# Performance work log

Hardware: AMD Instinct MI355X
Metric: run time of the kernel (lower is better)

Reference implementation:

```python
import jax, jax.numpy as jnp
import numpy as np

B, C, H, W = 16, 512, 32, 32
NUM_GROUPS = 32
EPS = 1e-5


def setup_inputs() -> dict:
    key = jax.random.key(0)
    ks = jax.random.split(key, 7)
    x = jax.random.normal(ks[0], (B, C, H, W), dtype=jnp.float32)
    gamma = jnp.ones((C,), dtype=jnp.float32)
    beta = jnp.zeros((C,), dtype=jnp.float32)
    # project_in: Conv2d(C, 3C, 1) -> weight [3C, C], bias [3C]
    w_in = jax.random.normal(ks[1], (3 * C, C), dtype=jnp.float32) / np.sqrt(C)
    b_in = jnp.zeros((3 * C,), dtype=jnp.float32)
    # project_out: Conv2d(C, C, 1) with init_scale=0.0 -> zero-init in original;
    # use small random weights so gradients/outputs are non-trivial for testing.
    w_out = jax.random.normal(ks[2], (C, C), dtype=jnp.float32) / np.sqrt(C)
    b_out = jnp.zeros((C,), dtype=jnp.float32)
    return {"x": x, "gamma": gamma, "beta": beta, "w_in": w_in, "b_in": b_in,
            "w_out": w_out, "b_out": b_out}


def group_norm(x, gamma, beta):
    b, c, h, w = x.shape
    xg = x.reshape(b, NUM_GROUPS, c // NUM_GROUPS, h, w)
    mean = xg.mean(axis=(2, 3, 4), keepdims=True)
    var = xg.var(axis=(2, 3, 4), keepdims=True)
    xn = ((xg - mean) * jax.lax.rsqrt(var + EPS)).reshape(b, c, h, w)
    return xn * gamma[None, :, None, None] + beta[None, :, None, None]


def reference(x, gamma, beta, w_in, b_in, w_out, b_out):
    skip = x  # in_channels == out_channels -> Identity skip
    xn = group_norm(x, gamma, beta)
    # 1x1 conv == channel matmul
    qkv = jnp.einsum('oc,bchw->bohw', w_in, xn) + b_in[None, :, None, None]
    q, k, v = jnp.split(qkv, 3, axis=1)  # each [B, C, H, W]
    cm = q.shape[1]
    # [B, H, W, H*W] scores
    scores = jnp.einsum('bchw,bcHW->bhwHW', q, k).reshape(B, H, W, H * W)
    attn = jax.nn.softmax(scores / jnp.sqrt(jnp.float32(cm)), axis=-1)
    attn = attn.reshape(B, H, W, H, W)
    out = jnp.einsum('bhwHW,bcHW->bchw', attn, v)
    out = jnp.einsum('oc,bchw->bohw', w_out, out) + b_out[None, :, None, None]
    return out + skip
```

## Files before the change

kernel.cpp:

```cpp
#include <hip/hip_runtime.h>
#include <hip/hip_bf16.h>
#include <cstdint>
#include <cstddef>

#define HW   1024
#define NC   512
#define NB   16
#define EPSV 1e-5f

typedef __hip_bfloat16 bf16;
typedef __attribute__((ext_vector_type(8))) __bf16 bf16x8;
typedef __attribute__((ext_vector_type(4))) float f32x4;

__device__ __forceinline__ float b2f(bf16 h) { return __bfloat162float(h); }

__device__ __forceinline__ void gload16(const void* g, void* l) {
  __builtin_amdgcn_global_load_lds(
      (const __attribute__((address_space(1))) uint32_t*)g,
      (__attribute__((address_space(3))) uint32_t*)l, 16, 0, 0);
}

__global__ __launch_bounds__(256) void cvt_w_kernel(
    const float* __restrict__ wi, const float* __restrict__ wo,
    bf16* __restrict__ wib, bf16* __restrict__ wob) {
  int i = blockIdx.x * 256 + threadIdx.x;
  const float4* src;
  bf16* dst;
  int j;
  if (i < 196608) { src = (const float4*)wi; j = i; dst = wib; }
  else            { src = (const float4*)wo; j = i - 196608; dst = wob; }
  float4 v = src[j];
  union { bf16 h[4]; uint2 u; } p;
  p.h[0] = __float2bfloat16(v.x); p.h[1] = __float2bfloat16(v.y);
  p.h[2] = __float2bfloat16(v.z); p.h[3] = __float2bfloat16(v.w);
  *(uint2*)&dst[(size_t)j * 4] = p.u;
}

__global__ __launch_bounds__(256) void gn_kernel(
    const float* __restrict__ x, const float* __restrict__ gamma,
    const float* __restrict__ beta, bf16* __restrict__ xn) {
  int blk = blockIdx.x;
  int b = blk >> 5, g = blk & 31;
  size_t base = ((size_t)(b * NC + g * 16)) * HW;
  const float4* src4 = (const float4*)(x + base);
  int t = threadIdx.x;
  float s = 0.f, ss = 0.f;
  float4 v[16];
#pragma unroll
  for (int i = 0; i < 16; ++i) {
    v[i] = src4[t + i * 256];
    s  += v[i].x + v[i].y + v[i].z + v[i].w;
    ss += v[i].x * v[i].x + v[i].y * v[i].y + v[i].z * v[i].z + v[i].w * v[i].w;
  }
  __shared__ float red[256];
  red[t] = s; __syncthreads();
  for (int o = 128; o > 0; o >>= 1) { if (t < o) red[t] += red[t + o]; __syncthreads(); }
  float mean = red[0] * (1.f / 16384.f);
  __syncthreads();
  red[t] = ss; __syncthreads();
  for (int o = 128; o > 0; o >>= 1) { if (t < o) red[t] += red[t + o]; __syncthreads(); }
  float var = red[0] * (1.f / 16384.f) - mean * mean;
  float rstd = rsqrtf(var + EPSV);

  __shared__ bf16 sm[16][1032];
#pragma unroll
  for (int i = 0; i < 16; ++i) {
    int idx = t + i * 256;
    int c = idx >> 8;
    int hw4 = (idx & 255) * 4;
    float gm = gamma[g * 16 + c], bt = beta[g * 16 + c];
    union { bf16 h[4]; uint2 u; } p;
    p.h[0] = __float2bfloat16((v[i].x - mean) * rstd * gm + bt);
    p.h[1] = __float2bfloat16((v[i].y - mean) * rstd * gm + bt);
    p.h[2] = __float2bfloat16((v[i].z - mean) * rstd * gm + bt);
    p.h[3] = __float2bfloat16((v[i].w - mean) * rstd * gm + bt);
    *(uint2*)&sm[c][hw4] = p.u;
  }
  __syncthreads();
  bf16* dst = xn + (size_t)b * HW * NC + g * 16;
#pragma unroll
  for (int it = 0; it < 8; ++it) {
    int u = it * 256 + t;
    int hw = u >> 1;
    int c8 = (u & 1) * 8;
    union { bf16 h[8]; uint4 q; } p;
#pragma unroll
    for (int j = 0; j < 8; ++j) p.h[j] = sm[c8 + j][hw];
    *(uint4*)&dst[(size_t)hw * NC + c8] = p.q;
  }
}

template <int MODE>
__global__ __launch_bounds__(256) void gemm_bt(
    const bf16* __restrict__ A, int lda, long long sA,
    const bf16* __restrict__ B, int ldb, long long sB,
    void* __restrict__ Cv, int ldc, long long sC,
    int K,
    const float* __restrict__ bias) {
  __shared__ bf16 sT[2][128][32];
  int z = blockIdx.z;
  const bf16* Ab = A + (size_t)z * sA;
  const bf16* Bb = B + (size_t)z * sB;
  int n0 = blockIdx.x * 128, m0 = blockIdx.y * 128;
  int t = threadIdx.x;
  int l = t & 63, w = t >> 6;
  int wm = w >> 1, wn = w & 1;

  int srow = t >> 2;
  int scol = (t & 3) * 8;

  f32x4 acc[4][4] = {};

  const bf16* ga0 = Ab + (size_t)(m0 + srow) * lda + scol;
  const bf16* gb0 = Bb + (size_t)(n0 + srow) * ldb + scol;

  for (int k0 = 0; k0 < K; k0 += 32) {
    gload16(ga0 + k0, &sT[0][srow][scol]);
    gload16(ga0 + (size_t)64 * lda + k0, &sT[0][64 + srow][scol]);
    gload16(gb0 + k0, &sT[1][srow][scol]);
    gload16(gb0 + (size_t)64 * ldb + k0, &sT[1][64 + srow][scol]);
    __syncthreads();
    bf16x8 af[4], bfr[4];
    int kc = (l >> 4) * 8;
    int ra = wm * 64 + (l & 15);
    int rb = wn * 64 + (l & 15);
#pragma unroll
    for (int i = 0; i < 4; ++i) {
      af[i]  = *(const bf16x8*)&sT[0][ra + i * 16][kc];
      bfr[i] = *(const bf16x8*)&sT[1][rb + i * 16][kc];
    }
#pragma unroll
    for (int i = 0; i < 4; ++i)
#pragma unroll
      for (int j = 0; j < 4; ++j)
        acc[i][j] = __builtin_amdgcn_mfma_f32_16x16x32_bf16(af[i], bfr[j], acc[i][j], 0, 0, 0);
    __syncthreads();
  }

  int rbase = (l >> 4) * 4;
#pragma unroll
  for (int i = 0; i < 4; ++i) {
    int row = m0 + wm * 64 + i * 16 + rbase;
    float4 bv = make_float4(0.f, 0.f, 0.f, 0.f);
    if (MODE == 0) bv = *(const float4*)&bias[row];
    else if (MODE == 1) { if (bias) bv = *(const float4*)&bias[row]; }
#pragma unroll
    for (int j = 0; j < 4; ++j) {
      int col = n0 + wn * 64 + j * 16 + (l & 15);
      if (MODE == 0) {
        bf16* C = (bf16*)Cv + (size_t)z * sC;
        union { bf16 h[4]; uint2 u; } p;
        p.h[0] = __float2bfloat16(acc[i][j][0] + bv.x);
        p.h[1] = __float2bfloat16(acc[i][j][1] + bv.y);
        p.h[2] = __float2bfloat16(acc[i][j][2] + bv.z);
        p.h[3] = __float2bfloat16(acc[i][j][3] + bv.w);
        *(uint2*)&C[(size_t)col * ldc + row] = p.u;
      } else {
        bf16* C = (bf16*)Cv + (size_t)z * sC;
        float bb[4] = {bv.x, bv.y, bv.z, bv.w};
#pragma unroll
        for (int r = 0; r < 4; ++r)
          C[(size_t)(row + r) * ldc + col] = __float2bfloat16(acc[i][j][r] + bb[r]);
      }
    }
  }
}

__global__ __launch_bounds__(512, 1) void flash_kernel(
    const bf16* __restrict__ qk, const bf16* __restrict__ vcm,
    const bf16* __restrict__ wout, const float* __restrict__ b_out,
    const float* __restrict__ x, float* __restrict__ out) {
  __shared__ char lds[163840];
  char* Qs  = lds;
  char* Kb0 = lds + 65536;
  char* Kb1 = lds + 81920;
  char* Vs  = lds + 98304;
  char* Wb0 = lds + 65536;
  char* Wb1 = lds + 98304;
  float* redl = (float*)(lds + 131072);

  int id = blockIdx.x;
  int xcd = id & 7, rest = id >> 3;
  int q = rest & 15, bh = rest >> 4;
  int b = xcd + bh * 8;
  int i0 = q * 64;

  const char* qkC = (const char*)qk + (size_t)b * 2097152;
  const char* vC  = (const char*)vcm + (size_t)b * 1048576;
  const char* wC  = (const char*)wout;

  int t = threadIdx.x, l = t & 63, w = t >> 6;
  int l15 = l & 15, lq = l >> 4;
  int jg = w >> 1, ih = w & 1;
  int chb = w * 64;

  auto stage_k = [&](int tile_, int p_, char* dst_) {
#pragma unroll
    for (int qq = 0; qq < 2; ++qq) {
      int A = qq * 8192 + t * 16;
      int jh = A >> 12, k2 = (A >> 10) & 3, jlo = (A >> 6) & 15, cb = A & 63;
      gload16(qkC + (size_t)(tile_ * 64 + jh * 16 + jlo) * 2048 + 1024
                  + p_ * 256 + k2 * 64 + cb,
              dst_ + A);
    }
  };
  auto stage_v = [&](int tile_, int v_) {
    int chh = t >> 7, js = (t >> 6) & 1, cl = (t >> 2) & 15, jb = (t & 3) * 16;
    int ch = v_ * 64 + chh * 16 + cl;
    gload16(vC + (size_t)ch * 2048 + tile_ * 128 + js * 64 + jb,
            Vs + v_ * 8192 + t * 16);
  };
  auto stage_w = [&](int kc_, char* dst_) {
#pragma unroll
    for (int it = 0; it < 4; ++it) {
      int A = it * 8192 + t * 16;
      int coh = A >> 10, col = (A >> 6) & 15, cb = A & 63;
      gload16(wC + (size_t)(coh * 16 + col) * 1024 + kc_ * 64 + cb, dst_ + A);
    }
  };

  {
#pragma unroll
    for (int it = 0; it < 8; ++it) {
      int A = it * 8192 + t * 16;
      int ih2 = A >> 14, ks = (A >> 10) & 15, ilo = (A >> 6) & 15, cb = A & 63;
      gload16(qkC + (size_t)(i0 + ih2 * 16 + ilo) * 2048 + ks * 64 + cb, Qs + A);
    }
  }
  stage_k(0, 0, Kb0);

  float lacc[2] = {0.f, 0.f};
  f32x4 o[4][4] = {};
  const float scl = 0.044194173824159216f;

  __syncthreads();

  for (int tile = 0; tile < 16; ++tile) {
    char* PsBuf = (tile & 1) ? Kb1 : Kb0;
    f32x4 s[2] = {};
#pragma unroll
    for (int p = 0; p < 4; ++p) {
      if (p < 3) {
        char* kd = ((p + 1 + tile) & 1) ? Kb1 : Kb0;
        stage_k(tile, p + 1, kd);
      }
      stage_v(tile, p * 2);
      stage_v(tile, p * 2 + 1);
      const char* kcur = ((p + tile) & 1) ? Kb1 : Kb0;
#pragma unroll
      for (int k2 = 0; k2 < 4; ++k2) {
        bf16x8 kf = *(const bf16x8*)(kcur + jg * 4096 + k2 * 1024 + l15 * 64 + lq * 16);
#pragma unroll
        for (int ni = 0; ni < 2; ++ni) {
          bf16x8 qf = *(const bf16x8*)(Qs + (ih * 2 + ni) * 16384
                        + (p * 4 + k2) * 1024 + l15 * 64 + lq * 16);
          s[ni] = __builtin_amdgcn_mfma_f32_16x16x32_bf16(kf, qf, s[ni], 0, 0, 0);
        }
      }
      __syncthreads();
    }
#pragma unroll
    for (int ni = 0; ni < 2; ++ni) {
      int i = ih * 32 + ni * 16 + l15;
      float p0 = __expf(s[ni][0] * scl);
      float p1 = __expf(s[ni][1] * scl);
      float p2 = __expf(s[ni][2] * scl);
      float p3 = __expf(s[ni][3] * scl);
      lacc[ni] += p0 + p1 + p2 + p3;
      union { bf16 h[4]; uint64_t u; } pk;
      pk.h[0] = __float2bfloat16(p0); pk.h[1] = __float2bfloat16(p1);
      pk.h[2] = __float2bfloat16(p2); pk.h[3] = __float2bfloat16(p3);
      int dst = (ih * 2 + ni) * 2048 + (jg >> 1) * 1024 + l15 * 64
              + (jg & 1) * 32 + lq * 8;
      *(uint64_t*)(PsBuf + dst) = pk.u;
      (void)i;
    }
    __syncthreads();
    if (tile < 15) {
      char* kd = ((tile + 1) & 1) ? Kb1 : Kb0;
      stage_k(tile + 1, 0, kd);
    }
#pragma unroll
    for (int ks = 0; ks < 2; ++ks) {
      bf16x8 vf[4];
#pragma unroll
      for (int mi = 0; mi < 4; ++mi)
        vf[mi] = *(const bf16x8*)(Vs + (w * 4 + mi) * 2048 + ks * 1024
                   + l15 * 64 + lq * 16);
#pragma unroll
      for (int ni = 0; ni < 4; ++ni) {
        bf16x8 pf = *(const bf16x8*)(PsBuf + ni * 2048 + ks * 1024
                      + l15 * 64 + lq * 16);
#pragma unroll
        for (int mi = 0; mi < 4; ++mi)
          o[mi][ni] = __builtin_amdgcn_mfma_f32_16x16x32_bf16(vf[mi], pf, o[mi][ni], 0, 0, 0);
      }
    }
    __syncthreads();
  }

  stage_w(0, Wb0);
#pragma unroll
  for (int ni = 0; ni < 2; ++ni) {
    float v = lacc[ni];
    v += __shfl_xor(v, 16);
    v += __shfl_xor(v, 32);
    if (l < 16) redl[jg * 64 + ih * 32 + ni * 16 + l] = v;
  }
  __syncthreads();
  float linv[4];
#pragma unroll
  for (int ni = 0; ni < 4; ++ni) {
    int i = ni * 16 + l15;
    linv[ni] = 1.f / (redl[i] + redl[64 + i] + redl[128 + i] + redl[192 + i]);
  }
#pragma unroll
  for (int mi = 0; mi < 4; ++mi)
#pragma unroll
    for (int ni = 0; ni < 4; ++ni) {
      union { bf16 h[4]; uint64_t u; } pk;
#pragma unroll
      for (int r = 0; r < 4; ++r)
        pk.h[r] = __float2bfloat16(o[mi][ni][r] * linv[ni]);
      int dst = ni * 16384 + (w * 2 + (mi >> 1)) * 1024 + l15 * 64
              + (mi & 1) * 32 + lq * 8;
      *(uint64_t*)(Qs + dst) = pk.u;
    }
  __syncthreads();

  f32x4 acc2[4][4] = {};
#pragma unroll
  for (int kc = 0; kc < 16; ++kc) {
    if (kc < 15) stage_w(kc + 1, ((kc + 1) & 1) ? Wb1 : Wb0);
    const char* Wc = (kc & 1) ? Wb1 : Wb0;
    bf16x8 wf[4];
#pragma unroll
    for (int mi = 0; mi < 4; ++mi)
      wf[mi] = *(const bf16x8*)(Wc + (w * 4 + mi) * 1024 + l15 * 64 + lq * 16);
#pragma unroll
    for (int ni = 0; ni < 4; ++ni) {
      bf16x8 pf = *(const bf16x8*)(Qs + ni * 16384 + kc * 1024
                    + l15 * 64 + lq * 16);
#pragma unroll
      for (int mi = 0; mi < 4; ++mi)
        acc2[mi][ni] = __builtin_amdgcn_mfma_f32_16x16x32_bf16(wf[mi], pf, acc2[mi][ni], 0, 0, 0);
    }
    __syncthreads();
  }

  const float* xb = x + (size_t)b * 524288;
  float* ob = out + (size_t)b * 524288;
#pragma unroll
  for (int mi = 0; mi < 4; ++mi) {
    int cbase = chb + mi * 16 + lq * 4;
    float4 bv = *(const float4*)&b_out[cbase];
    float bb[4] = {bv.x, bv.y, bv.z, bv.w};
#pragma unroll
    for (int ni = 0; ni < 4; ++ni) {
      int i = i0 + ni * 16 + l15;
#pragma unroll
      for (int r = 0; r < 4; ++r) {
        size_t off = (size_t)(cbase + r) * 1024 + i;
        ob[off] = acc2[mi][ni][r] + bb[r] + xb[off];
      }
    }
  }
}

extern "C" void kernel_launch(void* const* d_in, const int* in_sizes, int n_in,
                              void* d_out, int out_size, void* d_ws, size_t ws_size,
                              hipStream_t stream) {
  const float* x     = (const float*)d_in[0];
  const float* gamma = (const float*)d_in[1];
  const float* beta  = (const float*)d_in[2];
  const float* w_in  = (const float*)d_in[3];
  const float* b_in  = (const float*)d_in[4];
  const float* w_out = (const float*)d_in[5];
  const float* b_out = (const float*)d_in[6];
  float* out = (float*)d_out;

  char* w = (char*)d_ws;
  bf16* xn  = (bf16*)w;
  bf16* qk  = (bf16*)(w + ((size_t)16 << 20));
  bf16* vcm = (bf16*)(w + ((size_t)48 << 20));
  bf16* wib = (bf16*)(w + ((size_t)64 << 20));
  bf16* wob = (bf16*)(w + ((size_t)64 << 20) + ((size_t)3 << 19));

  cvt_w_kernel<<<1024, 256, 0, stream>>>(w_in, w_out, wib, wob);
  gn_kernel<<<NB * 32, 256, 0, stream>>>(x, gamma, beta, xn);

  gemm_bt<0><<<dim3(8, 8, NB), 256, 0, stream>>>(
      wib, 512, 0, xn, 512, 512 * 1024, qk, 1024, 1024 * 1024, 512, b_in);
  gemm_bt<1><<<dim3(8, 4, NB), 256, 0, stream>>>(
      wib + 1024 * 512, 512, 0, xn, 512, 512 * 1024, vcm, 1024, 512 * 1024, 512,
      b_in + 1024);

  flash_kernel<<<256, 512, 0, stream>>>(qk, vcm, wob, b_out, x, out);
}
```

Baseline: 151.7 us.

## Pre-swizzle K, V and W_out into MFMA fragment layouts and load them directly

The QKV projection epilogues now write K, V and the converted output-projection weight straight into MFMA-fragment-ordered layouts. The attention kernel can then read operand fragments from global memory into registers instead of staging them through LDS with barriers. The key loop is reorganised into 8 tiles of 128 keys, with each wave owning one 16-key slice, and LDS use drops from 160KB to 96KB. The cost is uncoalesced scattered stores in the GEMM epilogues (MODE 5 writes single bf16 elements) and reliance on cache/latency hiding for direct global fragment loads in the hot loop.

```diff
diff --git a/kernel.cpp b/kernel.cpp
--- a/kernel.cpp
+++ b/kernel.cpp
@@ -12,8 +12,6 @@
 typedef __attribute__((ext_vector_type(8))) __bf16 bf16x8;
 typedef __attribute__((ext_vector_type(4))) float f32x4;
 
-__device__ __forceinline__ float b2f(bf16 h) { return __bfloat162float(h); }
-
 __device__ __forceinline__ void gload16(const void* g, void* l) {
   __builtin_amdgcn_global_load_lds(
       (const __attribute__((address_space(1))) uint32_t*)g,
@@ -22,18 +20,25 @@
 
 __global__ __launch_bounds__(256) void cvt_w_kernel(
     const float* __restrict__ wi, const float* __restrict__ wo,
-    bf16* __restrict__ wib, bf16* __restrict__ wob) {
+    bf16* __restrict__ wib, char* __restrict__ wobf) {
   int i = blockIdx.x * 256 + threadIdx.x;
-  const float4* src;
-  bf16* dst;
-  int j;
-  if (i < 196608) { src = (const float4*)wi; j = i; dst = wib; }
-  else            { src = (const float4*)wo; j = i - 196608; dst = wob; }
-  float4 v = src[j];
-  union { bf16 h[4]; uint2 u; } p;
-  p.h[0] = __float2bfloat16(v.x); p.h[1] = __float2bfloat16(v.y);
-  p.h[2] = __float2bfloat16(v.z); p.h[3] = __float2bfloat16(v.w);
-  *(uint2*)&dst[(size_t)j * 4] = p.u;
+  if (i < 196608) {
+    float4 v = ((const float4*)wi)[i];
+    union { bf16 h[4]; uint2 u; } p;
+    p.h[0] = __float2bfloat16(v.x); p.h[1] = __float2bfloat16(v.y);
+    p.h[2] = __float2bfloat16(v.z); p.h[3] = __float2bfloat16(v.w);
+    *(uint2*)&wib[(size_t)i * 4] = p.u;
+  } else {
+    int j = i - 196608;
+    float4 v = ((const float4*)wo)[j];
+    int elem = j * 4;
+    int co = elem >> 9, c = elem & 511;
+    union { bf16 h[4]; uint2 u; } p;
+    p.h[0] = __float2bfloat16(v.x); p.h[1] = __float2bfloat16(v.y);
+    p.h[2] = __float2bfloat16(v.z); p.h[3] = __float2bfloat16(v.w);
+    int chh = co >> 4, col_ = co & 15, kc = c >> 5, cc = c & 31;
+    *(uint2*)(wobf + (((chh * 16 + kc) << 10) + col_ * 64 + cc * 2)) = p.u;
+  }
 }
 
 __global__ __launch_bounds__(256) void gn_kernel(
@@ -141,43 +146,50 @@
 #pragma unroll
   for (int i = 0; i < 4; ++i) {
     int row = m0 + wm * 64 + i * 16 + rbase;
-    float4 bv = make_float4(0.f, 0.f, 0.f, 0.f);
-    if (MODE == 0) bv = *(const float4*)&bias[row];
-    else if (MODE == 1) { if (bias) bv = *(const float4*)&bias[row]; }
+    float4 bv = *(const float4*)&bias[row];
+    float bb[4] = {bv.x, bv.y, bv.z, bv.w};
 #pragma unroll
     for (int j = 0; j < 4; ++j) {
       int col = n0 + wn * 64 + j * 16 + (l & 15);
       if (MODE == 0) {
         bf16* C = (bf16*)Cv + (size_t)z * sC;
         union { bf16 h[4]; uint2 u; } p;
-        p.h[0] = __float2bfloat16(acc[i][j][0] + bv.x);
-        p.h[1] = __float2bfloat16(acc[i][j][1] + bv.y);
-        p.h[2] = __float2bfloat16(acc[i][j][2] + bv.z);
-        p.h[3] = __float2bfloat16(acc[i][j][3] + bv.w);
+#pragma unroll
+        for (int r = 0; r < 4; ++r) p.h[r] = __float2bfloat16(acc[i][j][r] + bb[r]);
         *(uint2*)&C[(size_t)col * ldc + row] = p.u;
+      } else if (MODE == 4) {
+        char* C = (char*)Cv + (size_t)z * sC * 2;
+        int tile = col >> 7, jgc = (col >> 4) & 7, j_lo = col & 15;
+        int kw = row >> 5, cc = row & 31;
+        union { bf16 h[4]; uint2 u; } p;
+#pragma unroll
+        for (int r = 0; r < 4; ++r) p.h[r] = __float2bfloat16(acc[i][j][r] + bb[r]);
+        *(uint2*)(C + (((tile * 8 + jgc) * 16 + kw) << 10) + j_lo * 64 + cc * 2) = p.u;
       } else {
-        bf16* C = (bf16*)Cv + (size_t)z * sC;
-        float bb[4] = {bv.x, bv.y, bv.z, bv.w};
-#pragma unroll
-        for (int r = 0; r < 4; ++r)
-          C[(size_t)(row + r) * ldc + col] = __float2bfloat16(acc[i][j][r] + bb[r]);
+        char* C = (char*)Cv + (size_t)z * sC * 2;
+        int tile = col >> 7, jj = col & 127;
+        int ks = jj >> 5, jc = jj & 31;
+#pragma unroll
+        for (int r = 0; r < 4; ++r) {
+          int ch = row + r;
+          int chh = ch >> 4, chl = ch & 15;
+          *(bf16*)(C + (((tile * 32 + chh) * 4 + ks) << 10)
+                     + chl * 64 + jc * 2) = __float2bfloat16(acc[i][j][r] + bb[r]);
+        }
       }
     }
   }
 }
 
 __global__ __launch_bounds__(512, 1) void flash_kernel(
-    const bf16* __restrict__ qk, const bf16* __restrict__ vcm,
-    const bf16* __restrict__ wout, const float* __restrict__ b_out,
-    const float* __restrict__ x, float* __restrict__ out) {
-  __shared__ char lds[163840];
-  char* Qs  = lds;
-  char* Kb0 = lds + 65536;
-  char* Kb1 = lds + 81920;
-  char* Vs  = lds + 98304;
-  char* Wb0 = lds + 65536;
-  char* Wb1 = lds + 98304;
-  float* redl = (float*)(lds + 131072);
+    const bf16* __restrict__ qtok, const bf16* __restrict__ kfrag,
+    const bf16* __restrict__ vfrag, const bf16* __restrict__ wfrag,
+    const float* __restrict__ b_out, const float* __restrict__ x,
+    float* __restrict__ out) {
+  __shared__ char lds[98304];
+  char* Qs = lds;
+  char* Ps = lds + 65536;
+  float* redl = (float*)(lds + 65536);
 
   int id = blockIdx.x;
   int xcd = id & 7, rest = id >> 3;
@@ -185,83 +197,51 @@
   int b = xcd + bh * 8;
   int i0 = q * 64;
 
-  const char* qkC = (const char*)qk + (size_t)b * 2097152;
-  const char* vC  = (const char*)vcm + (size_t)b * 1048576;
-  const char* wC  = (const char*)wout;
+  const char* qC = (const char*)qtok + (size_t)b * 1048576;
+  const char* kC = (const char*)kfrag + (size_t)b * 1048576;
+  const char* vC = (const char*)vfrag + (size_t)b * 1048576;
+  const char* wC = (const char*)wfrag;
 
   int t = threadIdx.x, l = t & 63, w = t >> 6;
   int l15 = l & 15, lq = l >> 4;
-  int jg = w >> 1, ih = w & 1;
+  int fofs = l15 * 64 + lq * 16;
   int chb = w * 64;
 
-  auto stage_k = [&](int tile_, int p_, char* dst_) {
-#pragma unroll
-    for (int qq = 0; qq < 2; ++qq) {
-      int A = qq * 8192 + t * 16;
-      int jh = A >> 12, k2 = (A >> 10) & 3, jlo = (A >> 6) & 15, cb = A & 63;
-      gload16(qkC + (size_t)(tile_ * 64 + jh * 16 + jlo) * 2048 + 1024
-                  + p_ * 256 + k2 * 64 + cb,
-              dst_ + A);
-    }
-  };
-  auto stage_v = [&](int tile_, int v_) {
-    int chh = t >> 7, js = (t >> 6) & 1, cl = (t >> 2) & 15, jb = (t & 3) * 16;
-    int ch = v_ * 64 + chh * 16 + cl;
-    gload16(vC + (size_t)ch * 2048 + tile_ * 128 + js * 64 + jb,
-            Vs + v_ * 8192 + t * 16);
-  };
-  auto stage_w = [&](int kc_, char* dst_) {
-#pragma unroll
-    for (int it = 0; it < 4; ++it) {
-      int A = it * 8192 + t * 16;
-      int coh = A >> 10, col = (A >> 6) & 15, cb = A & 63;
-      gload16(wC + (size_t)(coh * 16 + col) * 1024 + kc_ * 64 + cb, dst_ + A);
-    }
-  };
-
-  {
-#pragma unroll
-    for (int it = 0; it < 8; ++it) {
-      int A = it * 8192 + t * 16;
-      int ih2 = A >> 14, ks = (A >> 10) & 15, ilo = (A >> 6) & 15, cb = A & 63;
-      gload16(qkC + (size_t)(i0 + ih2 * 16 + ilo) * 2048 + ks * 64 + cb, Qs + A);
-    }
-  }
-  stage_k(0, 0, Kb0);
-
-  float lacc[2] = {0.f, 0.f};
+#pragma unroll
+  for (int it = 0; it < 8; ++it) {
+    int A = it * 8192 + t * 16;
+    int ih2 = A >> 14, ks = (A >> 10) & 15, ilo = (A >> 6) & 15, cb = A & 63;
+    gload16(qC + (size_t)(i0 + ih2 * 16 + ilo) * 1024 + ks * 64 + cb, Qs + A);
+  }
+
+  float lacc[4] = {0.f, 0.f, 0.f, 0.f};
   f32x4 o[4][4] = {};
   const float scl = 0.044194173824159216f;
 
   __syncthreads();
 
-  for (int tile = 0; tile < 16; ++tile) {
-    char* PsBuf = (tile & 1) ? Kb1 : Kb0;
-    f32x4 s[2] = {};
-#pragma unroll
-    for (int p = 0; p < 4; ++p) {
-      if (p < 3) {
-        char* kd = ((p + 1 + tile) & 1) ? Kb1 : Kb0;
-        stage_k(tile, p + 1, kd);
+  for (int tile = 0; tile < 8; ++tile) {
+    char* Pc = Ps + (tile & 1) * 16384;
+    bf16x8 vf[4][4];
+#pragma unroll
+    for (int ks = 0; ks < 4; ++ks)
+#pragma unroll
+      for (int mi = 0; mi < 4; ++mi)
+        vf[ks][mi] = *(const bf16x8*)(vC
+            + (((size_t)(tile * 32 + (w * 4 + mi)) * 4 + ks) << 10) + fofs);
+    f32x4 s[4] = {};
+#pragma unroll
+    for (int kw = 0; kw < 16; ++kw) {
+      bf16x8 kf = *(const bf16x8*)(kC
+          + (((size_t)(tile * 8 + w) * 16 + kw) << 10) + fofs);
+#pragma unroll
+      for (int ni = 0; ni < 4; ++ni) {
+        bf16x8 qf = *(const bf16x8*)(Qs + ni * 16384 + kw * 1024 + fofs);
+        s[ni] = __builtin_amdgcn_mfma_f32_16x16x32_bf16(kf, qf, s[ni], 0, 0, 0);
       }
-      stage_v(tile, p * 2);
-      stage_v(tile, p * 2 + 1);
-      const char* kcur = ((p + tile) & 1) ? Kb1 : Kb0;
-#pragma unroll
-      for (int k2 = 0; k2 < 4; ++k2) {
-        bf16x8 kf = *(const bf16x8*)(kcur + jg * 4096 + k2 * 1024 + l15 * 64 + lq * 16);
-#pragma unroll
-        for (int ni = 0; ni < 2; ++ni) {
-          bf16x8 qf = *(const bf16x8*)(Qs + (ih * 2 + ni) * 16384
-                        + (p * 4 + k2) * 1024 + l15 * 64 + lq * 16);
-          s[ni] = __builtin_amdgcn_mfma_f32_16x16x32_bf16(kf, qf, s[ni], 0, 0, 0);
-        }
-      }
-      __syncthreads();
-    }
-#pragma unroll
-    for (int ni = 0; ni < 2; ++ni) {
-      int i = ih * 32 + ni * 16 + l15;
+    }
+#pragma unroll
+    for (int ni = 0; ni < 4; ++ni) {
       float p0 = __expf(s[ni][0] * scl);
       float p1 = __expf(s[ni][1] * scl);
       float p2 = __expf(s[ni][2] * scl);
@@ -270,49 +250,37 @@
       union { bf16 h[4]; uint64_t u; } pk;
       pk.h[0] = __float2bfloat16(p0); pk.h[1] = __float2bfloat16(p1);
       pk.h[2] = __float2bfloat16(p2); pk.h[3] = __float2bfloat16(p3);
-      int dst = (ih * 2 + ni) * 2048 + (jg >> 1) * 1024 + l15 * 64
-              + (jg & 1) * 32 + lq * 8;
-      *(uint64_t*)(PsBuf + dst) = pk.u;
-      (void)i;
+      *(uint64_t*)(Pc + ni * 4096 + (w >> 1) * 1024 + l15 * 64
+                   + (w & 1) * 32 + lq * 8) = pk.u;
     }
     __syncthreads();
-    if (tile < 15) {
-      char* kd = ((tile + 1) & 1) ? Kb1 : Kb0;
-      stage_k(tile + 1, 0, kd);
-    }
-#pragma unroll
-    for (int ks = 0; ks < 2; ++ks) {
-      bf16x8 vf[4];
-#pragma unroll
-      for (int mi = 0; mi < 4; ++mi)
-        vf[mi] = *(const bf16x8*)(Vs + (w * 4 + mi) * 2048 + ks * 1024
-                   + l15 * 64 + lq * 16);
+#pragma unroll
+    for (int ks = 0; ks < 4; ++ks)
 #pragma unroll
       for (int ni = 0; ni < 4; ++ni) {
-        bf16x8 pf = *(const bf16x8*)(PsBuf + ni * 2048 + ks * 1024
-                      + l15 * 64 + lq * 16);
+        bf16x8 pf = *(const bf16x8*)(Pc + ni * 4096 + ks * 1024 + fofs);
 #pragma unroll
         for (int mi = 0; mi < 4; ++mi)
-          o[mi][ni] = __builtin_amdgcn_mfma_f32_16x16x32_bf16(vf[mi], pf, o[mi][ni], 0, 0, 0);
+          o[mi][ni] = __builtin_amdgcn_mfma_f32_16x16x32_bf16(vf[ks][mi], pf, o[mi][ni], 0, 0, 0);
       }
-    }
-    __syncthreads();
-  }
-
-  stage_w(0, Wb0);
-#pragma unroll
-  for (int ni = 0; ni < 2; ++ni) {
+  }
+
+#pragma unroll
+  for (int ni = 0; ni < 4; ++ni) {
     float v = lacc[ni];
     v += __shfl_xor(v, 16);
     v += __shfl_xor(v, 32);
-    if (l < 16) redl[jg * 64 + ih * 32 + ni * 16 + l] = v;
+    if (l < 16) redl[w * 64 + ni * 16 + l] = v;
   }
   __syncthreads();
   float linv[4];
 #pragma unroll
   for (int ni = 0; ni < 4; ++ni) {
     int i = ni * 16 + l15;
-    linv[ni] = 1.f / (redl[i] + redl[64 + i] + redl[128 + i] + redl[192 + i]);
+    float v = redl[i];
+#pragma unroll
+    for (int w2 = 1; w2 < 8; ++w2) v += redl[w2 * 64 + i];
+    linv[ni] = 1.f / v;
   }
 #pragma unroll
   for (int mi = 0; mi < 4; ++mi)
@@ -331,21 +299,17 @@
   f32x4 acc2[4][4] = {};
 #pragma unroll
   for (int kc = 0; kc < 16; ++kc) {
-    if (kc < 15) stage_w(kc + 1, ((kc + 1) & 1) ? Wb1 : Wb0);
-    const char* Wc = (kc & 1) ? Wb1 : Wb0;
     bf16x8 wf[4];
 #pragma unroll
     for (int mi = 0; mi < 4; ++mi)
-      wf[mi] = *(const bf16x8*)(Wc + (w * 4 + mi) * 1024 + l15 * 64 + lq * 16);
+      wf[mi] = *(const bf16x8*)(wC + (((size_t)(w * 4 + mi) * 16 + kc) << 10) + fofs);
 #pragma unroll
     for (int ni = 0; ni < 4; ++ni) {
-      bf16x8 pf = *(const bf16x8*)(Qs + ni * 16384 + kc * 1024
-                    + l15 * 64 + lq * 16);
+      bf16x8 pf = *(const bf16x8*)(Qs + ni * 16384 + kc * 1024 + fofs);
 #pragma unroll
       for (int mi = 0; mi < 4; ++mi)
         acc2[mi][ni] = __builtin_amdgcn_mfma_f32_16x16x32_bf16(wf[mi], pf, acc2[mi][ni], 0, 0, 0);
     }
-    __syncthreads();
   }
 
   const float* xb = x + (size_t)b * 524288;
@@ -380,20 +344,25 @@
   float* out = (float*)d_out;
 
   char* w = (char*)d_ws;
-  bf16* xn  = (bf16*)w;
-  bf16* qk  = (bf16*)(w + ((size_t)16 << 20));
-  bf16* vcm = (bf16*)(w + ((size_t)48 << 20));
-  bf16* wib = (bf16*)(w + ((size_t)64 << 20));
-  bf16* wob = (bf16*)(w + ((size_t)64 << 20) + ((size_t)3 << 19));
-
-  cvt_w_kernel<<<1024, 256, 0, stream>>>(w_in, w_out, wib, wob);
+  bf16* xn    = (bf16*)w;
+  bf16* qtok  = (bf16*)(w + ((size_t)16 << 20));
+  bf16* kfrag = (bf16*)(w + ((size_t)32 << 20));
+  bf16* vfrag = (bf16*)(w + ((size_t)48 << 20));
+  bf16* wib   = (bf16*)(w + ((size_t)64 << 20));
+  char* wobf  = (char*)(w + ((size_t)64 << 20) + ((size_t)3 << 19));
+
+  cvt_w_kernel<<<1024, 256, 0, stream>>>(w_in, w_out, wib, wobf);
   gn_kernel<<<NB * 32, 256, 0, stream>>>(x, gamma, beta, xn);
 
-  gemm_bt<0><<<dim3(8, 8, NB), 256, 0, stream>>>(
-      wib, 512, 0, xn, 512, 512 * 1024, qk, 1024, 1024 * 1024, 512, b_in);
-  gemm_bt<1><<<dim3(8, 4, NB), 256, 0, stream>>>(
-      wib + 1024 * 512, 512, 0, xn, 512, 512 * 1024, vcm, 1024, 512 * 1024, 512,
+  gemm_bt<0><<<dim3(8, 4, NB), 256, 0, stream>>>(
+      wib, 512, 0, xn, 512, 512 * 1024, qtok, 512, 512 * 1024, 512, b_in);
+  gemm_bt<4><<<dim3(8, 4, NB), 256, 0, stream>>>(
+      wib + 512 * 512, 512, 0, xn, 512, 512 * 1024, kfrag, 0, 512 * 1024, 512,
+      b_in + 512);
+  gemm_bt<5><<<dim3(8, 4, NB), 256, 0, stream>>>(
+      wib + 1024 * 512, 512, 0, xn, 512, 512 * 1024, vfrag, 0, 512 * 1024, 512,
       b_in + 1024);
 
-  flash_kernel<<<256, 512, 0, stream>>>(qk, vcm, wob, b_out, x, out);
-}
+  flash_kernel<<<256, 512, 0, stream>>>(qtok, kfrag, vfrag, (const bf16*)wobf,
+                                        b_out, x, out);
+}
```

Result: faster. 142.9 us (-5.8%).
